# Kernel tuning notes

Measured on AMD Instinct MI355X. Metric: run time of the kernel, lower is better.

The kernel has to match this reference:

```python
import jax, jax.numpy as jnp
import numpy as np

B, C, H, W = 2, 192, 48, 512
EMB, HEADS, DOUT, MAXM, THR, EPS = 64, 2, 192, 64, 0.01, 1e-5
DV = DOUT // HEADS  # per-head value dim (96)


def setup_inputs() -> dict:
    key = jax.random.key(0)
    ks = jax.random.split(key, 16)
    s = 0.02
    inp = {
        "l": jax.random.normal(ks[0], (B, C, H, W), jnp.float32),
        "r": jax.random.normal(ks[1], (B, C, H, W), jnp.float32),
        "ln_l_g": jnp.ones((C,), jnp.float32),
        "ln_l_b": jnp.zeros((C,), jnp.float32),
        "ln_r_g": jnp.ones((C,), jnp.float32),
        "ln_r_b": jnp.zeros((C,), jnp.float32),
    }
    ki = 2
    for p in ("rtl", "ltr"):
        inp[p + "_wq"] = jax.random.normal(ks[ki], (HEADS * EMB, C, 3), jnp.float32) * s; ki += 1
        inp[p + "_bq"] = jnp.zeros((HEADS * EMB,), jnp.float32)
        inp[p + "_wk"] = jax.random.normal(ks[ki], (HEADS * EMB, C, 3), jnp.float32) * s; ki += 1
        inp[p + "_bk"] = jnp.zeros((HEADS * EMB,), jnp.float32)
        inp[p + "_wv"] = jax.random.normal(ks[ki], (DOUT, C, 3), jnp.float32) * s; ki += 1
        inp[p + "_bv"] = jnp.zeros((DOUT,), jnp.float32)
        inp[p + "_wo"] = jax.random.normal(ks[ki], (DOUT, DOUT), jnp.float32) * s; ki += 1
        inp[p + "_bo"] = jnp.zeros((DOUT,), jnp.float32)
    inp["ffl_w"] = jax.random.normal(ks[ki], (DOUT, DOUT), jnp.float32) * s; ki += 1
    inp["ffl_b"] = jnp.zeros((DOUT,), jnp.float32)
    inp["ffr_w"] = jax.random.normal(ks[ki], (DOUT, DOUT), jnp.float32) * s; ki += 1
    inp["ffr_b"] = jnp.zeros((DOUT,), jnp.float32)
    return inp


def _layernorm(x, g, b):
    m = x.mean(-1, keepdims=True)
    v = x.var(-1, keepdims=True)
    return (x - m) / jnp.sqrt(v + EPS) * g + b


def _conv1d(x, w, b):
    # x: [N, Cin, L], w: [Cout, Cin, 3], same padding
    y = jax.lax.conv_general_dilated(x, w, (1,), [(1, 1)], dimension_numbers=("NCH", "OIH", "NCH"))
    return y + b[None, :, None]


def _conv_attn(q_seq, k_seq, v_seq, wq, bq, wk, bk, wv, bv, wo, bo, mask):
    # q_seq/k_seq/v_seq: [N, L, C]; mask: [L, L] bool (True = masked)
    N, L, _ = q_seq.shape
    Q = _conv1d(q_seq.transpose(0, 2, 1), wq, bq).reshape(N, HEADS, EMB, L).transpose(0, 1, 3, 2)  # b h l d
    K = _conv1d(k_seq.transpose(0, 2, 1), wk, bk).reshape(N, HEADS, EMB, L).transpose(0, 1, 3, 2)
    V = _conv1d(v_seq.transpose(0, 2, 1), wv, bv).reshape(N, HEADS, DV, L).transpose(0, 1, 3, 2)
    A = jnp.einsum("bhqd,bhkd->bhqk", Q, K) / np.sqrt(EMB).astype(np.float32)
    A = jnp.where(mask, -jnp.inf, A)
    A = jax.nn.softmax(A, axis=-1)
    A = A * (A > THR)  # valid_mask thresholding after softmax
    O = jnp.einsum("bhqk,bhkd->bhqd", A, V)
    O = O.transpose(0, 2, 1, 3).reshape(N, L, DOUT)
    return jnp.einsum("nld,od->nlo", O, wo) + bo, A


def reference(l, r, ln_l_g, ln_l_b, ln_r_g, ln_r_b,
              rtl_wq, rtl_bq, rtl_wk, rtl_bk, rtl_wv, rtl_bv, rtl_wo, rtl_bo,
              ltr_wq, ltr_bq, ltr_wk, ltr_bk, ltr_wv, ltr_bv, ltr_wo, ltr_bo,
              ffl_w, ffl_b, ffr_w, ffr_b):
    ls = l.transpose(0, 2, 3, 1).reshape(B * H, W, C)  # (b h) w c
    rs = r.transpose(0, 2, 3, 1).reshape(B * H, W, C)
    ln_ = _layernorm(ls, ln_l_g, ln_l_b)
    rn_ = _layernorm(rs, ln_r_g, ln_r_b)
    i = jnp.arange(W)[:, None]
    j = jnp.arange(W)[None, :]
    mask_left = (j < i) | (j - i > MAXM)   # left query i attends keys j in [i, i+MAXM]
    mask_right = (j > i) | (i - j > MAXM)  # right query i attends keys j in [i-MAXM, i]
    l_mha, A_rtl = _conv_attn(ln_, rn_, rs, rtl_wq, rtl_bq, rtl_wk, rtl_bk, rtl_wv, rtl_bv, rtl_wo, rtl_bo, mask_left)
    r_mha, A_ltr = _conv_attn(rn_, ln_, ls, ltr_wq, ltr_bq, ltr_wk, ltr_bk, ltr_wv, ltr_bv, ltr_wo, ltr_bo, mask_right)
    lo = ls + l_mha
    ro = rs + r_mha
    lo = lo + (jnp.einsum("nwc,oc->nwo", lo, ffl_w) + ffl_b)
    ro = ro + (jnp.einsum("nwc,oc->nwo", ro, ffr_w) + ffr_b)
    l_out = lo.reshape(B, H, W, C).transpose(0, 3, 1, 2)
    r_out = ro.reshape(B, H, W, C).transpose(0, 3, 1, 2)
    return (l_out, r_out, A_rtl, A_ltr)
```

## Files before the change

### kernel.cpp

```cpp
#include <hip/hip_runtime.h>
#include <cstddef>
#include <cstdint>

constexpr int kC = 192;
constexpr int kW = 512;
constexpr int kHH = 48;

typedef unsigned short u16;
typedef __attribute__((ext_vector_type(8))) short bf16x8;
typedef __attribute__((ext_vector_type(4))) float f32x4;
typedef __attribute__((ext_vector_type(4))) unsigned short us4;

__device__ inline u16 f2bf(float f) {
  union { float f; uint32_t u; } v; v.f = f;
  uint32_t r = v.u + 0x7FFF + ((v.u >> 16) & 1);
  return (u16)(r >> 16);
}
__device__ inline float bf2f(u16 u) {
  return __uint_as_float(((uint32_t)u) << 16);
}

__global__ void __launch_bounds__(256) ln_kernel(
    const float* __restrict__ xl, const float* __restrict__ xr,
    const float* __restrict__ gl, const float* __restrict__ bl,
    const float* __restrict__ gr, const float* __restrict__ br,
    u16* __restrict__ lnl, u16* __restrict__ lraw,
    u16* __restrict__ lnr, u16* __restrict__ rraw) {
  int n = blockIdx.y;
  int w0 = blockIdx.x * 64;
  int side = blockIdx.z;
  const float* x = side ? xr : xl;
  const float* g = side ? gr : gl;
  const float* b = side ? br : bl;
  u16* lnout = side ? lnr : lnl;
  u16* rawout = side ? rraw : lraw;
  int bb = n / kHH, h = n % kHH;
  __shared__ float tile[64][193];
  __shared__ float red[8][64];
  __shared__ float mean_s[64], rstd_s[64];
  int tid = threadIdx.x;
  int lane = tid & 63, wv = tid >> 6;
  for (int c = wv; c < kC; c += 4)
    tile[lane][c] = x[(((size_t)bb * kC + c) * kHH + h) * kW + w0 + lane];
  __syncthreads();
  {
    int w = tid & 63, part = tid >> 6;
    float s = 0.f, s2 = 0.f;
    const float* row = &tile[w][0];
    for (int c = part * 48; c < part * 48 + 48; ++c) {
      float v = row[c];
      s += v; s2 += v * v;
    }
    red[part][w] = s;
    red[part + 4][w] = s2;
  }
  __syncthreads();
  if (tid < 64) {
    float s = red[0][tid] + red[1][tid] + red[2][tid] + red[3][tid];
    float s2 = red[4][tid] + red[5][tid] + red[6][tid] + red[7][tid];
    float m = s * (1.f / 192.f);
    float var = s2 * (1.f / 192.f) - m * m;
    mean_s[tid] = m;
    rstd_s[tid] = rsqrtf(var + 1e-5f);
  }
  __syncthreads();
  for (int u = tid; u < 64 * 48; u += 256) {
    int w = u / 48, c4 = (u % 48) * 4;
    float mm = mean_s[w], rs = rstd_s[w];
    us4 lp, rp;
#pragma unroll
    for (int j = 0; j < 4; ++j) {
      float raw = tile[w][c4 + j];
      rp[j] = f2bf(raw);
      lp[j] = f2bf((raw - mm) * rs * g[c4 + j] + b[c4 + j]);
    }
    size_t idx = ((size_t)n * kW + w0 + w) * kC + c4;
    *reinterpret_cast<us4*>(&lnout[idx]) = lp;
    *reinterpret_cast<us4*>(&rawout[idx]) = rp;
  }
}

__global__ void wprep_all(
    const float* wq0, const float* wk0, const float* wv0,
    const float* wq1, const float* wk1, const float* wv1,
    const float* bq0, const float* bk0, const float* bv0,
    const float* bq1, const float* bk1, const float* bv1,
    const float* wo0, const float* wo1, const float* fw0, const float* fw1,
    u16* __restrict__ wall, u16* __restrict__ pfw, float* __restrict__ ball) {
  int idx = blockIdx.x * 256 + threadIdx.x;
  if (idx < 516096) {
    int dir = idx / 258048, off = idx % 258048;
    const float* src; int soff;
    if (off < 73728) { src = dir ? wq1 : wq0; soff = off; }
    else if (off < 147456) { src = dir ? wk1 : wk0; soff = off - 73728; }
    else { src = dir ? wv1 : wv0; soff = off - 147456; }
    int o = soff / 576, k = soff % 576, t = k / 192, c = k % 192;
    wall[idx] = f2bf(src[((size_t)o * kC + c) * 3 + t]);
  } else if (idx < 516096 + 147456) {
    int i2 = idx - 516096;
    int mat = i2 / 36864, off = i2 % 36864;
    const float* src = mat == 0 ? wo0 : mat == 1 ? wo1 : mat == 2 ? fw0 : fw1;
    pfw[i2] = f2bf(src[off]);
  } else if (idx < 516096 + 147456 + 896) {
    int bi = idx - 516096 - 147456;
    int dir = bi / 448, boff = bi % 448;
    const float* s; int so;
    if (boff < 128) { s = dir ? bq1 : bq0; so = boff; }
    else if (boff < 256) { s = dir ? bk1 : bk0; so = boff - 128; }
    else { s = dir ? bv1 : bv0; so = boff - 256; }
    ball[bi] = s[so];
  }
}

template <int NF>
__device__ __forceinline__ void conv_core(
    const u16* __restrict__ in, const u16* __restrict__ w2,
    int n, int l0, u16* As, f32x4 (&acc)[4][NF]) {
  int tid = threadIdx.x;
  int wid = tid >> 6, lane = tid & 63;
  int wm = wid >> 1, wn = wid & 1;
  int lr = lane & 15, g = lane >> 4;
  for (int u = tid; u < 130 * 48; u += 256) {
    int row = u / 48, q = u % 48;
    int l = l0 - 1 + row;
    us4 v = {0, 0, 0, 0};
    if (l >= 0 && l < kW)
      v = *reinterpret_cast<const us4*>(in + ((size_t)n * kW + l) * kC + q * 4);
    *reinterpret_cast<us4*>(&As[row * 200 + q * 4]) = v;
  }
  __syncthreads();
  const u16* wbase = w2 + (size_t)(wn * NF * 16 + lr) * 576 + g * 8;
#pragma unroll
  for (int t = 0; t < 3; ++t) {
#pragma unroll
    for (int c0 = 0; c0 < 192; c0 += 64) {
#pragma unroll
      for (int ks = 0; ks < 2; ++ks) {
        bf16x8 a[4], b[NF];
#pragma unroll
        for (int mf = 0; mf < 4; ++mf)
          a[mf] = *reinterpret_cast<const bf16x8*>(
              &As[(wm * 64 + mf * 16 + lr + t) * 200 + c0 + ks * 32 + g * 8]);
#pragma unroll
        for (int nf = 0; nf < NF; ++nf)
          b[nf] = *reinterpret_cast<const bf16x8*>(
              wbase + (size_t)nf * 16 * 576 + t * 192 + c0 + ks * 32);
#pragma unroll
        for (int mf = 0; mf < 4; ++mf)
#pragma unroll
          for (int nf = 0; nf < NF; ++nf)
            acc[mf][nf] = __builtin_amdgcn_mfma_f32_16x16x32_bf16(a[mf], b[nf], acc[mf][nf], 0, 0, 0);
      }
    }
  }
}

__global__ void __launch_bounds__(256) conv_qk(
    const u16* __restrict__ lnl, const u16* __restrict__ lnr,
    const u16* __restrict__ wall, const float* __restrict__ ball,
    u16* __restrict__ Qbf, u16* __restrict__ Kbf) {
  int l0 = blockIdx.x * 128;
  int jid = blockIdx.y;
  int n = blockIdx.z;
  int dir = jid >> 1, which = jid & 1;
  const u16* in = which == 0 ? (dir ? lnr : lnl) : (dir ? lnl : lnr);
  const u16* w2 = wall + (size_t)dir * 258048 + which * 73728;
  const float* bias = ball + dir * 448 + which * 128;

  __shared__ __attribute__((aligned(16))) u16 As[130 * 200];
  f32x4 acc[4][4] = {};
  conv_core<4>(in, w2, n, l0, As, acc);

  int tid = threadIdx.x;
  int wid = tid >> 6, lane = tid & 63;
  int wm = wid >> 1, wn = wid & 1;
  int lr = lane & 15, g = lane >> 4;
  u16* outp = (which == 0 ? Qbf : Kbf) + (size_t)dir * 6291456;
#pragma unroll
  for (int nf = 0; nf < 4; ++nf) {
    int o = wn * 64 + nf * 16 + lr;
    int hh = o >> 6, e = o & 63;
    float bsv = bias[o];
#pragma unroll
    for (int mf = 0; mf < 4; ++mf) {
#pragma unroll
      for (int rg = 0; rg < 4; ++rg) {
        int l = l0 + wm * 64 + mf * 16 + g * 4 + rg;
        outp[((size_t)(n * 2 + hh) * kW + l) * 64 + e] = f2bf(acc[mf][nf][rg] + bsv);
      }
    }
  }
}

__global__ void __launch_bounds__(256) conv_v(
    const u16* __restrict__ lraw, const u16* __restrict__ rraw,
    const u16* __restrict__ wall, const float* __restrict__ ball,
    u16* __restrict__ Vbf) {
  int l0 = blockIdx.x * 128;
  int dir = blockIdx.y;
  int n = blockIdx.z;
  const u16* in = dir ? lraw : rraw;
  const u16* w2 = wall + (size_t)dir * 258048 + 147456;
  const float* bias = ball + dir * 448 + 256;

  __shared__ __attribute__((aligned(16))) u16 As[130 * 200];
  f32x4 acc[4][6] = {};
  conv_core<6>(in, w2, n, l0, As, acc);

  int tid = threadIdx.x;
  int wid = tid >> 6, lane = tid & 63;
  int wm = wid >> 1, wn = wid & 1;
  int lr = lane & 15, g = lane >> 4;
  u16* outp = Vbf + (size_t)dir * 9437184;
#pragma unroll
  for (int nf = 0; nf < 6; ++nf) {
    int e = nf * 16 + lr;
    float bsv = bias[wn * 96 + e];
#pragma unroll
    for (int mf = 0; mf < 4; ++mf) {
      int lb = l0 + wm * 64 + mf * 16 + g * 4;
      us4 p;
#pragma unroll
      for (int rg = 0; rg < 4; ++rg) p[rg] = f2bf(acc[mf][nf][rg] + bsv);
      *reinterpret_cast<us4*>(&outp[((size_t)(n * 2 + wn) * 96 + e) * kW + lb]) = p;
    }
  }
}

__global__ void __launch_bounds__(256) attn_mfma(
    const u16* __restrict__ Qbf, const u16* __restrict__ Kbf,
    const u16* __restrict__ Vbf, float* __restrict__ Abase,
    u16* __restrict__ Obf) {
  int qb = blockIdx.x;
  int nh = blockIdx.y;
  int dir = blockIdx.z;
  int q0 = qb * 64;
  int k_start = dir == 0 ? q0 : (q0 >= 64 ? q0 - 64 : 0);
  int k_end = dir == 0 ? (q0 + 128 <= kW ? q0 + 128 : kW) : q0 + 64;
  int kfr = (k_end - k_start) >> 4;
  const u16* Q = Qbf + ((size_t)dir * 192 + nh) * kW * 64;
  const u16* K = Kbf + ((size_t)dir * 192 + nh) * kW * 64;
  const u16* V = Vbf + ((size_t)dir * 192 + nh) * 96 * kW;
  float* Aout = Abase + (size_t)dir * 50331648 + (size_t)nh * kW * kW;
  u16* Obase = Obf + (size_t)dir * 9437184;

  __shared__ __attribute__((aligned(16))) u16 smem[26880];
  u16* Qs = smem;
  u16* Ks = smem + 4608;
  u16* Ps = smem;
  u16* Vt = smem + 13824;

  int tid = threadIdx.x;
  int wid = tid >> 6, lane = tid & 63;
  int lr = lane & 15, g = lane >> 4;

  for (int u = tid; u < 64 * 16; u += 256) {
    int row = u >> 4, c4 = (u & 15) * 4;
    *reinterpret_cast<us4*>(&Qs[row * 72 + c4]) =
        *reinterpret_cast<const us4*>(&Q[(size_t)(q0 + row) * 64 + c4]);
  }
  for (int u = tid; u < 128 * 16; u += 256) {
    int row = u >> 4, c4 = (u & 15) * 4;
    *reinterpret_cast<us4*>(&Ks[row * 72 + c4]) =
        *reinterpret_cast<const us4*>(&K[(size_t)(k_start + row) * 64 + c4]);
  }
  for (int u = tid; u < 96 * 32; u += 256) {
    int row = u >> 5, c4 = (u & 31) * 4;
    *reinterpret_cast<us4*>(&Vt[row * 136 + c4]) =
        *reinterpret_cast<const us4*>(&V[(size_t)row * kW + k_start + c4]);
  }
  __syncthreads();

  f32x4 sT[8];
#pragma unroll
  for (int kf = 0; kf < 8; ++kf) sT[kf] = f32x4{0.f, 0.f, 0.f, 0.f};
#pragma unroll
  for (int kc = 0; kc < 2; ++kc) {
    bf16x8 bq = *reinterpret_cast<const bf16x8*>(&Qs[(wid * 16 + lr) * 72 + kc * 32 + g * 8]);
#pragma unroll
    for (int kf = 0; kf < 8; ++kf) {
      bf16x8 ak = *reinterpret_cast<const bf16x8*>(&Ks[(kf * 16 + lr) * 72 + kc * 32 + g * 8]);
      sT[kf] = __builtin_amdgcn_mfma_f32_16x16x32_bf16(ak, bq, sT[kf], 0, 0, 0);
    }
  }

  int i = q0 + wid * 16 + lr;
  float mx = -INFINITY;
#pragma unroll
  for (int kf = 0; kf < 8; ++kf) {
#pragma unroll
    for (int r = 0; r < 4; ++r) {
      int jj = k_start + kf * 16 + g * 4 + r;
      bool valid = (jj < k_end) &&
                   (dir == 0 ? (jj >= i && jj - i <= 64) : (jj <= i && i - jj <= 64));
      float v = valid ? sT[kf][r] * 0.125f : -INFINITY;
      sT[kf][r] = v;
      mx = fmaxf(mx, v);
    }
  }
  mx = fmaxf(mx, __shfl_xor(mx, 16));
  mx = fmaxf(mx, __shfl_xor(mx, 32));
  float ssum = 0.f;
#pragma unroll
  for (int kf = 0; kf < 8; ++kf) {
#pragma unroll
    for (int r = 0; r < 4; ++r) {
      float e = __expf(sT[kf][r] - mx);
      sT[kf][r] = e;
      ssum += e;
    }
  }
  ssum += __shfl_xor(ssum, 16);
  ssum += __shfl_xor(ssum, 32);
  float inv = 1.f / ssum;

  __syncthreads();

  {
    float* arow = Aout + (size_t)i * kW + k_start;
#pragma unroll
    for (int kf = 0; kf < 8; ++kf) {
      f32x4 pv;
      us4 pb;
#pragma unroll
      for (int r = 0; r < 4; ++r) {
        float p = sT[kf][r] * inv;
        p = (p > 0.01f) ? p : 0.f;
        pv[r] = p;
        pb[r] = f2bf(p);
      }
      *reinterpret_cast<us4*>(&Ps[(wid * 16 + lr) * 136 + kf * 16 + g * 4]) = pb;
      if (kf < kfr)
        __builtin_nontemporal_store(pv, reinterpret_cast<f32x4*>(arow + kf * 16 + g * 4));
    }
  }
  {
    int row = tid >> 2, t4 = tid & 3;
    f32x4 z4 = {0.f, 0.f, 0.f, 0.f};
    float* arow = Aout + (size_t)(q0 + row) * kW;
    for (int c4 = t4; c4 < (k_start >> 2); c4 += 4)
      __builtin_nontemporal_store(z4, reinterpret_cast<f32x4*>(arow + c4 * 4));
    for (int c4 = (k_end >> 2) + t4; c4 < 128; c4 += 4)
      __builtin_nontemporal_store(z4, reinterpret_cast<f32x4*>(arow + c4 * 4));
  }
  __syncthreads();

  f32x4 oacc[6];
#pragma unroll
  for (int ef = 0; ef < 6; ++ef) oacc[ef] = f32x4{0.f, 0.f, 0.f, 0.f};
#pragma unroll
  for (int kc = 0; kc < 4; ++kc) {
    bf16x8 ap = *reinterpret_cast<const bf16x8*>(&Ps[(wid * 16 + lr) * 136 + kc * 32 + g * 8]);
#pragma unroll
    for (int ef = 0; ef < 6; ++ef) {
      bf16x8 bv = *reinterpret_cast<const bf16x8*>(&Vt[(ef * 16 + lr) * 136 + kc * 32 + g * 8]);
      oacc[ef] = __builtin_amdgcn_mfma_f32_16x16x32_bf16(ap, bv, oacc[ef], 0, 0, 0);
    }
  }
  __syncthreads();
  u16* Os2 = smem;
#pragma unroll
  for (int ef = 0; ef < 6; ++ef) {
    int e = ef * 16 + lr;
#pragma unroll
    for (int r = 0; r < 4; ++r)
      Os2[(wid * 16 + g * 4 + r) * 104 + e] = f2bf(oacc[ef][r]);
  }
  __syncthreads();
  int n_ = nh >> 1, h_ = nh & 1;
  for (int u = tid; u < 64 * 24; u += 256) {
    int q = u / 24, c4 = (u % 24) * 4;
    *reinterpret_cast<us4*>(&Obase[((size_t)n_ * kW + q0 + q) * kC + h_ * 96 + c4]) =
        *reinterpret_cast<const us4*>(&Os2[q * 104 + c4]);
  }
}

__global__ void __launch_bounds__(256) projff_mfma(
    const u16* __restrict__ pfw,
    const float* __restrict__ bo0, const float* __restrict__ bo1,
    const float* __restrict__ fb0, const float* __restrict__ fb1,
    const u16* __restrict__ Obf, const u16* __restrict__ lraw,
    const u16* __restrict__ rraw, float* __restrict__ outbase) {
  int l0 = blockIdx.x * 64;
  int z = blockIdx.y;
  int dir = z / 96, n = z % 96;
  const u16* wo2 = pfw + (dir ? 36864 : 0);
  const u16* fw2 = pfw + 73728 + (dir ? 36864 : 0);
  const float* bo_ = dir ? bo1 : bo0;
  const float* fb_ = dir ? fb1 : fb0;
  const u16* Osrc = Obf + (size_t)dir * 9437184;
  const u16* resbf = dir ? rraw : lraw;
  float* outb = outbase + (size_t)dir * 9437184;
  int bb = n / kHH, h = n % kHH;

  __shared__ __attribute__((aligned(16))) u16 Xs[64 * 200];
  __shared__ __attribute__((aligned(16))) u16 Rs[64 * 200];

  int tid = threadIdx.x;
  int wid = tid >> 6, lane = tid & 63;
  int wm = wid >> 1, wn = wid & 1;
  int lr = lane & 15, g = lane >> 4;

  for (int u = tid; u < 64 * 48; u += 256) {
    int row = u / 48, q = u % 48;
    size_t src = ((size_t)n * kW + l0 + row) * kC + q * 4;
    *reinterpret_cast<us4*>(&Xs[row * 200 + q * 4]) =
        *reinterpret_cast<const us4*>(&Osrc[src]);
    *reinterpret_cast<us4*>(&Rs[row * 200 + q * 4]) =
        *reinterpret_cast<const us4*>(&resbf[src]);
  }
  __syncthreads();

  const u16* wobase = wo2 + (size_t)(wn * 96 + lr) * kC + g * 8;
  const u16* fwbase = fw2 + (size_t)(wn * 96 + lr) * kC + g * 8;

  f32x4 accp[2][6] = {};
#pragma unroll
  for (int c0 = 0; c0 < 192; c0 += 64) {
#pragma unroll
    for (int ks = 0; ks < 2; ++ks) {
      bf16x8 a[2], b[6];
#pragma unroll
      for (int m2 = 0; m2 < 2; ++m2)
        a[m2] = *reinterpret_cast<const bf16x8*>(
            &Xs[(wm * 32 + m2 * 16 + lr) * 200 + c0 + ks * 32 + g * 8]);
#pragma unroll
      for (int nf = 0; nf < 6; ++nf)
        b[nf] = *reinterpret_cast<const bf16x8*>(
            wobase + (size_t)nf * 16 * kC + c0 + ks * 32);
#pragma unroll
      for (int m2 = 0; m2 < 2; ++m2)
#pragma unroll
        for (int nf = 0; nf < 6; ++nf)
          accp[m2][nf] = __builtin_amdgcn_mfma_f32_16x16x32_bf16(a[m2], b[nf], accp[m2][nf], 0, 0, 0);
    }
  }
  __syncthreads();
#pragma unroll
  for (int nf = 0; nf < 6; ++nf) {
    int o = wn * 96 + nf * 16 + lr;
    float bv = bo_[o];
#pragma unroll
    for (int m2 = 0; m2 < 2; ++m2) {
#pragma unroll
      for (int r = 0; r < 4; ++r) {
        int l = wm * 32 + m2 * 16 + g * 4 + r;
        float v = accp[m2][nf][r] + bv + bf2f(Rs[l * 200 + o]);
        accp[m2][nf][r] = v;
        Xs[l * 200 + o] = f2bf(v);
      }
    }
  }
  __syncthreads();

  f32x4 accf[2][6] = {};
#pragma unroll
  for (int c0 = 0; c0 < 192; c0 += 64) {
#pragma unroll
    for (int ks = 0; ks < 2; ++ks) {
      bf16x8 a[2], b[6];
#pragma unroll
      for (int m2 = 0; m2 < 2; ++m2)
        a[m2] = *reinterpret_cast<const bf16x8*>(
            &Xs[(wm * 32 + m2 * 16 + lr) * 200 + c0 + ks * 32 + g * 8]);
#pragma unroll
      for (int nf = 0; nf < 6; ++nf)
        b[nf] = *reinterpret_cast<const bf16x8*>(
            fwbase + (size_t)nf * 16 * kC + c0 + ks * 32);
#pragma unroll
      for (int m2 = 0; m2 < 2; ++m2)
#pragma unroll
        for (int nf = 0; nf < 6; ++nf)
          accf[m2][nf] = __builtin_amdgcn_mfma_f32_16x16x32_bf16(a[m2], b[nf], accf[m2][nf], 0, 0, 0);
    }
  }
#pragma unroll
  for (int nf = 0; nf < 6; ++nf) {
    int o = wn * 96 + nf * 16 + lr;
    float bv = fb_[o];
#pragma unroll
    for (int m2 = 0; m2 < 2; ++m2) {
      f32x4 ov;
#pragma unroll
      for (int r = 0; r < 4; ++r)
        ov[r] = accf[m2][nf][r] + bv + accp[m2][nf][r];
      int l = l0 + wm * 32 + m2 * 16 + g * 4;
      *reinterpret_cast<f32x4*>(&outb[(((size_t)bb * kC + o) * kHH + h) * kW + l]) = ov;
    }
  }
}

extern "C" void kernel_launch(void* const* d_in, const int* in_sizes, int n_in,
                              void* d_out, int out_size, void* d_ws, size_t ws_size,
                              hipStream_t stream) {
  const float* l = (const float*)d_in[0];
  const float* r = (const float*)d_in[1];
  float* out = (float*)d_out;
  float* ws = (float*)d_ws;

  u16* lnl_bf  = (u16*)(ws + 0);
  u16* lnr_bf  = (u16*)(ws + 4718592);
  u16* lraw_bf = (u16*)(ws + 9437184);
  u16* rraw_bf = (u16*)(ws + 14155776);
  u16* wall    = (u16*)(ws + 18874368);
  float* ball  = ws + 19136512;
  u16* Qbf     = (u16*)(ws + 19137536);
  u16* Kbf     = (u16*)(ws + 25428992);
  u16* Vbf     = (u16*)(ws + 31720448);
  u16* Obf     = (u16*)(ws + 41157632);
  u16* pfw     = (u16*)(ws + 50594816);

  ln_kernel<<<dim3(8, 96, 2), 256, 0, stream>>>(
      l, r, (const float*)d_in[2], (const float*)d_in[3],
      (const float*)d_in[4], (const float*)d_in[5],
      lnl_bf, lraw_bf, lnr_bf, rraw_bf);

  wprep_all<<<(516096 + 147456 + 896 + 255) / 256, 256, 0, stream>>>(
      (const float*)d_in[6], (const float*)d_in[8], (const float*)d_in[10],
      (const float*)d_in[14], (const float*)d_in[16], (const float*)d_in[18],
      (const float*)d_in[7], (const float*)d_in[9], (const float*)d_in[11],
      (const float*)d_in[15], (const float*)d_in[17], (const float*)d_in[19],
      (const float*)d_in[12], (const float*)d_in[20],
      (const float*)d_in[22], (const float*)d_in[24],
      wall, pfw, ball);

  conv_qk<<<dim3(4, 4, 96), 256, 0, stream>>>(lnl_bf, lnr_bf, wall, ball, Qbf, Kbf);
  conv_v<<<dim3(4, 2, 96), 256, 0, stream>>>(lraw_bf, rraw_bf, wall, ball, Vbf);

  attn_mfma<<<dim3(8, 192, 2), 256, 0, stream>>>(
      Qbf, Kbf, Vbf, out + (size_t)18874368, Obf);

  projff_mfma<<<dim3(8, 192), 256, 0, stream>>>(
      pfw, (const float*)d_in[13], (const float*)d_in[21],
      (const float*)d_in[23], (const float*)d_in[25],
      Obf, lraw_bf, rraw_bf, out);
}
```

Before: 397.7 us.

## Merge prep kernels, offload attention zero-fill to conv kernels, skip masked MFMA tiles

Merges layernorm and weight preparation into one launch. Moves the zero-filling of the attention-probability outputs outside each band into extra blocks of the conv kernels, so those stores overlap with conv compute instead of running inside the attention kernel. Inside attention, skips QK and PV MFMA fragments that fall entirely outside each wave's band of valid keys. The zero-fill blocks run a per-element range check and must cover exactly the complement of what attention writes, which adds correctness risk.

Result: faster. 358.2 us (-9.9%).

```diff
diff --git a/kernel.cpp b/kernel.cpp
--- a/kernel.cpp
+++ b/kernel.cpp
@@ -20,15 +20,49 @@
   return __uint_as_float(((uint32_t)u) << 16);
 }
 
-__global__ void __launch_bounds__(256) ln_kernel(
+__global__ void __launch_bounds__(256) prep_kernel(
     const float* __restrict__ xl, const float* __restrict__ xr,
     const float* __restrict__ gl, const float* __restrict__ bl,
     const float* __restrict__ gr, const float* __restrict__ br,
     u16* __restrict__ lnl, u16* __restrict__ lraw,
-    u16* __restrict__ lnr, u16* __restrict__ rraw) {
-  int n = blockIdx.y;
-  int w0 = blockIdx.x * 64;
-  int side = blockIdx.z;
+    u16* __restrict__ lnr, u16* __restrict__ rraw,
+    const float* wq0, const float* wk0, const float* wv0,
+    const float* wq1, const float* wk1, const float* wv1,
+    const float* bq0, const float* bk0, const float* bv0,
+    const float* bq1, const float* bk1, const float* bv1,
+    const float* wo0, const float* wo1, const float* fw0, const float* fw1,
+    u16* __restrict__ wall, u16* __restrict__ pfw, float* __restrict__ ball) {
+  int bid = blockIdx.x;
+  int tid = threadIdx.x;
+  if (bid >= 1536) {
+    int idx = (bid - 1536) * 256 + tid;
+    if (idx < 516096) {
+      int dir = idx / 258048, off = idx % 258048;
+      const float* src; int soff;
+      if (off < 73728) { src = dir ? wq1 : wq0; soff = off; }
+      else if (off < 147456) { src = dir ? wk1 : wk0; soff = off - 73728; }
+      else { src = dir ? wv1 : wv0; soff = off - 147456; }
+      int o = soff / 576, k = soff % 576, t = k / 192, c = k % 192;
+      wall[idx] = f2bf(src[((size_t)o * kC + c) * 3 + t]);
+    } else if (idx < 516096 + 147456) {
+      int i2 = idx - 516096;
+      int mat = i2 / 36864, off = i2 % 36864;
+      const float* src = mat == 0 ? wo0 : mat == 1 ? wo1 : mat == 2 ? fw0 : fw1;
+      pfw[i2] = f2bf(src[off]);
+    } else if (idx < 516096 + 147456 + 896) {
+      int bi = idx - 516096 - 147456;
+      int dir = bi / 448, boff = bi % 448;
+      const float* s; int so;
+      if (boff < 128) { s = dir ? bq1 : bq0; so = boff; }
+      else if (boff < 256) { s = dir ? bk1 : bk0; so = boff - 128; }
+      else { s = dir ? bv1 : bv0; so = boff - 256; }
+      ball[bi] = s[so];
+    }
+    return;
+  }
+  int w0 = (bid & 7) * 64;
+  int n = (bid >> 3) % 96;
+  int side = bid / 768;
   const float* x = side ? xr : xl;
   const float* g = side ? gr : gl;
   const float* b = side ? br : bl;
@@ -38,7 +72,6 @@
   __shared__ float tile[64][193];
   __shared__ float red[8][64];
   __shared__ float mean_s[64], rstd_s[64];
-  int tid = threadIdx.x;
   int lane = tid & 63, wv = tid >> 6;
   for (int c = wv; c < kC; c += 4)
     tile[lane][c] = x[(((size_t)bb * kC + c) * kHH + h) * kW + w0 + lane];
@@ -77,38 +110,6 @@
     size_t idx = ((size_t)n * kW + w0 + w) * kC + c4;
     *reinterpret_cast<us4*>(&lnout[idx]) = lp;
     *reinterpret_cast<us4*>(&rawout[idx]) = rp;
-  }
-}
-
-__global__ void wprep_all(
-    const float* wq0, const float* wk0, const float* wv0,
-    const float* wq1, const float* wk1, const float* wv1,
-    const float* bq0, const float* bk0, const float* bv0,
-    const float* bq1, const float* bk1, const float* bv1,
-    const float* wo0, const float* wo1, const float* fw0, const float* fw1,
-    u16* __restrict__ wall, u16* __restrict__ pfw, float* __restrict__ ball) {
-  int idx = blockIdx.x * 256 + threadIdx.x;
-  if (idx < 516096) {
-    int dir = idx / 258048, off = idx % 258048;
-    const float* src; int soff;
-    if (off < 73728) { src = dir ? wq1 : wq0; soff = off; }
-    else if (off < 147456) { src = dir ? wk1 : wk0; soff = off - 73728; }
-    else { src = dir ? wv1 : wv0; soff = off - 147456; }
-    int o = soff / 576, k = soff % 576, t = k / 192, c = k % 192;
-    wall[idx] = f2bf(src[((size_t)o * kC + c) * 3 + t]);
-  } else if (idx < 516096 + 147456) {
-    int i2 = idx - 516096;
-    int mat = i2 / 36864, off = i2 % 36864;
-    const float* src = mat == 0 ? wo0 : mat == 1 ? wo1 : mat == 2 ? fw0 : fw1;
-    pfw[i2] = f2bf(src[off]);
-  } else if (idx < 516096 + 147456 + 896) {
-    int bi = idx - 516096 - 147456;
-    int dir = bi / 448, boff = bi % 448;
-    const float* s; int so;
-    if (boff < 128) { s = dir ? bq1 : bq0; so = boff; }
-    else if (boff < 256) { s = dir ? bk1 : bk0; so = boff - 128; }
-    else { s = dir ? bv1 : bv0; so = boff - 256; }
-    ball[bi] = s[so];
   }
 }
 
@@ -158,7 +159,24 @@
 __global__ void __launch_bounds__(256) conv_qk(
     const u16* __restrict__ lnl, const u16* __restrict__ lnr,
     const u16* __restrict__ wall, const float* __restrict__ ball,
-    u16* __restrict__ Qbf, u16* __restrict__ Kbf) {
+    u16* __restrict__ Qbf, u16* __restrict__ Kbf, float* __restrict__ A0) {
+  if (blockIdx.y == 4) {
+    int fid = blockIdx.z * 4 + blockIdx.x;
+    int base_row = fid * 256;
+    f32x4 z4 = {0.f, 0.f, 0.f, 0.f};
+    for (int u = threadIdx.x; u < 256 * 128; u += 256) {
+      int lrow = u >> 7, c4 = u & 127;
+      int rg = base_row + lrow;
+      int nh = rg >> 9, i = rg & 511;
+      int q0 = i & ~63;
+      int w1 = q0 + 128 > 512 ? 512 : q0 + 128;
+      int col = c4 * 4;
+      if (col < q0 || col >= w1)
+        __builtin_nontemporal_store(z4, reinterpret_cast<f32x4*>(
+            A0 + (size_t)nh * 262144 + (size_t)i * 512 + col));
+    }
+    return;
+  }
   int l0 = blockIdx.x * 128;
   int jid = blockIdx.y;
   int n = blockIdx.z;
@@ -195,7 +213,24 @@
 __global__ void __launch_bounds__(256) conv_v(
     const u16* __restrict__ lraw, const u16* __restrict__ rraw,
     const u16* __restrict__ wall, const float* __restrict__ ball,
-    u16* __restrict__ Vbf) {
+    u16* __restrict__ Vbf, float* __restrict__ A1) {
+  if (blockIdx.y == 2) {
+    int fid = blockIdx.z * 4 + blockIdx.x;
+    int base_row = fid * 256;
+    f32x4 z4 = {0.f, 0.f, 0.f, 0.f};
+    for (int u = threadIdx.x; u < 256 * 128; u += 256) {
+      int lrow = u >> 7, c4 = u & 127;
+      int rg = base_row + lrow;
+      int nh = rg >> 9, i = rg & 511;
+      int q0 = i & ~63;
+      int w0 = q0 >= 64 ? q0 - 64 : 0;
+      int col = c4 * 4;
+      if (col < w0 || col >= q0 + 64)
+        __builtin_nontemporal_store(z4, reinterpret_cast<f32x4*>(
+            A1 + (size_t)nh * 262144 + (size_t)i * 512 + col));
+    }
+    return;
+  }
   int l0 = blockIdx.x * 128;
   int dir = blockIdx.y;
   int n = blockIdx.z;
@@ -271,16 +306,23 @@
   }
   __syncthreads();
 
+  int lo_k = q0 + wid * 16 - (dir == 0 ? 0 : 64) - k_start;
+  int hi_k = q0 + wid * 16 + 15 + (dir == 0 ? 64 : 0) - k_start;
+
   f32x4 sT[8];
 #pragma unroll
   for (int kf = 0; kf < 8; ++kf) sT[kf] = f32x4{0.f, 0.f, 0.f, 0.f};
-#pragma unroll
-  for (int kc = 0; kc < 2; ++kc) {
-    bf16x8 bq = *reinterpret_cast<const bf16x8*>(&Qs[(wid * 16 + lr) * 72 + kc * 32 + g * 8]);
+  {
+    bf16x8 bq0 = *reinterpret_cast<const bf16x8*>(&Qs[(wid * 16 + lr) * 72 + g * 8]);
+    bf16x8 bq1 = *reinterpret_cast<const bf16x8*>(&Qs[(wid * 16 + lr) * 72 + 32 + g * 8]);
 #pragma unroll
     for (int kf = 0; kf < 8; ++kf) {
-      bf16x8 ak = *reinterpret_cast<const bf16x8*>(&Ks[(kf * 16 + lr) * 72 + kc * 32 + g * 8]);
-      sT[kf] = __builtin_amdgcn_mfma_f32_16x16x32_bf16(ak, bq, sT[kf], 0, 0, 0);
+      if (kf * 16 + 15 >= lo_k && kf * 16 <= hi_k) {
+        bf16x8 ak0 = *reinterpret_cast<const bf16x8*>(&Ks[(kf * 16 + lr) * 72 + g * 8]);
+        sT[kf] = __builtin_amdgcn_mfma_f32_16x16x32_bf16(ak0, bq0, sT[kf], 0, 0, 0);
+        bf16x8 ak1 = *reinterpret_cast<const bf16x8*>(&Ks[(kf * 16 + lr) * 72 + 32 + g * 8]);
+        sT[kf] = __builtin_amdgcn_mfma_f32_16x16x32_bf16(ak1, bq1, sT[kf], 0, 0, 0);
+      }
     }
   }
 
@@ -334,15 +376,6 @@
         __builtin_nontemporal_store(pv, reinterpret_cast<f32x4*>(arow + kf * 16 + g * 4));
     }
   }
-  {
-    int row = tid >> 2, t4 = tid & 3;
-    f32x4 z4 = {0.f, 0.f, 0.f, 0.f};
-    float* arow = Aout + (size_t)(q0 + row) * kW;
-    for (int c4 = t4; c4 < (k_start >> 2); c4 += 4)
-      __builtin_nontemporal_store(z4, reinterpret_cast<f32x4*>(arow + c4 * 4));
-    for (int c4 = (k_end >> 2) + t4; c4 < 128; c4 += 4)
-      __builtin_nontemporal_store(z4, reinterpret_cast<f32x4*>(arow + c4 * 4));
-  }
   __syncthreads();
 
   f32x4 oacc[6];
@@ -350,11 +383,13 @@
   for (int ef = 0; ef < 6; ++ef) oacc[ef] = f32x4{0.f, 0.f, 0.f, 0.f};
 #pragma unroll
   for (int kc = 0; kc < 4; ++kc) {
-    bf16x8 ap = *reinterpret_cast<const bf16x8*>(&Ps[(wid * 16 + lr) * 136 + kc * 32 + g * 8]);
-#pragma unroll
-    for (int ef = 0; ef < 6; ++ef) {
-      bf16x8 bv = *reinterpret_cast<const bf16x8*>(&Vt[(ef * 16 + lr) * 136 + kc * 32 + g * 8]);
-      oacc[ef] = __builtin_amdgcn_mfma_f32_16x16x32_bf16(ap, bv, oacc[ef], 0, 0, 0);
+    if (kc * 32 + 31 >= lo_k && kc * 32 <= hi_k) {
+      bf16x8 ap = *reinterpret_cast<const bf16x8*>(&Ps[(wid * 16 + lr) * 136 + kc * 32 + g * 8]);
+#pragma unroll
+      for (int ef = 0; ef < 6; ++ef) {
+        bf16x8 bv = *reinterpret_cast<const bf16x8*>(&Vt[(ef * 16 + lr) * 136 + kc * 32 + g * 8]);
+        oacc[ef] = __builtin_amdgcn_mfma_f32_16x16x32_bf16(ap, bv, oacc[ef], 0, 0, 0);
+      }
     }
   }
   __syncthreads();
@@ -510,12 +545,15 @@
   u16* Obf     = (u16*)(ws + 41157632);
   u16* pfw     = (u16*)(ws + 50594816);
 
-  ln_kernel<<<dim3(8, 96, 2), 256, 0, stream>>>(
+  float* A0 = out + (size_t)18874368;
+  float* A1 = out + (size_t)69206016;
+
+  int wp_items = 516096 + 147456 + 896;
+  int wp_blocks = (wp_items + 255) / 256;
+  prep_kernel<<<1536 + wp_blocks, 256, 0, stream>>>(
       l, r, (const float*)d_in[2], (const float*)d_in[3],
       (const float*)d_in[4], (const float*)d_in[5],
-      lnl_bf, lraw_bf, lnr_bf, rraw_bf);
-
-  wprep_all<<<(516096 + 147456 + 896 + 255) / 256, 256, 0, stream>>>(
+      lnl_bf, lraw_bf, lnr_bf, rraw_bf,
       (const float*)d_in[6], (const float*)d_in[8], (const float*)d_in[10],
       (const float*)d_in[14], (const float*)d_in[16], (const float*)d_in[18],
       (const float*)d_in[7], (const float*)d_in[9], (const float*)d_in[11],
@@ -524,11 +562,13 @@
       (const float*)d_in[22], (const float*)d_in[24],
       wall, pfw, ball);
 
-  conv_qk<<<dim3(4, 4, 96), 256, 0, stream>>>(lnl_bf, lnr_bf, wall, ball, Qbf, Kbf);
-  conv_v<<<dim3(4, 2, 96), 256, 0, stream>>>(lraw_bf, rraw_bf, wall, ball, Vbf);
+  conv_qk<<<dim3(4, 5, 96), 256, 0, stream>>>(
+      lnl_bf, lnr_bf, wall, ball, Qbf, Kbf, A0);
+  conv_v<<<dim3(4, 3, 96), 256, 0, stream>>>(
+      lraw_bf, rraw_bf, wall, ball, Vbf, A1);
 
   attn_mfma<<<dim3(8, 192, 2), 256, 0, stream>>>(
-      Qbf, Kbf, Vbf, out + (size_t)18874368, Obf);
+      Qbf, Kbf, Vbf, A0, Obf);
 
   projff_mfma<<<dim3(8, 192), 256, 0, stream>>>(
       pfw, (const float*)d_in[13], (const float*)d_in[21],
```
